# Optimization experiments

Measured on AMD Instinct MI355X. Metric: run time of the kernel, lower is better.

Reference implementation:

```python
import jax, jax.numpy as jnp
import numpy as np

NP, NA, H, K, TAU = 4096, 2048, 128, 5, 1.0
NODE_N = {'paper': NP, 'author': NA}
RELS = [('pp', 'paper', 'paper'), ('aa', 'author', 'author'),
        ('pa', 'paper', 'author'), ('ap', 'author', 'paper')]


def setup_inputs():
    key = jax.random.key(0)
    ks = jax.random.split(key, 32)
    f32 = jnp.float32
    def nrm(k, shape, scale=1.0):
        return jax.random.normal(k, shape, f32) * scale
    Epp, Eaa, Epa, Eap = 131072, 65536, 131072, 131072
    inp = {
        'x_paper': nrm(ks[0], (NP, H)),
        'x_author': nrm(ks[1], (NA, H)),
        'ei_pp': jax.random.randint(ks[2], (2, Epp), 0, NP, dtype=jnp.int32),
        'ei_aa': jax.random.randint(ks[3], (2, Eaa), 0, NA, dtype=jnp.int32),
        'ei_pa': jnp.stack([jax.random.randint(ks[4], (Epa,), 0, NP, dtype=jnp.int32),
                            jax.random.randint(ks[5], (Epa,), 0, NA, dtype=jnp.int32)]),
        'ei_ap': jnp.stack([jax.random.randint(ks[6], (Eap,), 0, NA, dtype=jnp.int32),
                            jax.random.randint(ks[7], (Eap,), 0, NP, dtype=jnp.int32)]),
        'batch_paper': jnp.zeros((NP,), jnp.int32),
        'batch_author': jnp.zeros((NA,), jnp.int32),
        'index': 7,
    }
    s = H ** -0.5
    i = 8
    for t in ('paper', 'author'):
        for l in (0, 1):
            inp['Wself_%s%d' % (t, l)] = nrm(ks[i], (H, H), s); i += 1
    for r, _, _ in RELS:
        for l in (0, 1):
            inp['W%s%d' % (r, l)] = nrm(ks[i], (H, H), s); i += 1
    for r in ('pp', 'aa'):
        inp['Wep1_%s' % r] = nrm(ks[i], (2 * H, 256), (2 * H) ** -0.5); i += 1
        inp['bep1_%s' % r] = jnp.zeros((256,), f32)
        inp['Wep2_%s' % r] = nrm(ks[i], (256, 2), 256 ** -0.5); i += 1
        inp['bep2_%s' % r] = jnp.zeros((2,), f32)
    inp['Wc'] = nrm(ks[i], (H, 5), s)
    inp['bc'] = jnp.zeros((5,), f32)
    return inp


def _mean_agg(msg, dst, n):
    s = jax.ops.segment_sum(msg, dst, num_segments=n)
    c = jax.ops.segment_sum(jnp.ones((msg.shape[0], 1), msg.dtype), dst, num_segments=n)
    return s / jnp.maximum(c, 1.0)


def _gnn(x, ei, p, single, edge_attn=None):
    # 2-layer relation-typed mean-aggregation hetero GNN.
    h = dict(x)
    for l in (0, 1):
        nh = {}
        for t in ('paper', 'author'):
            agg = h[t] @ p['Wself_%s%d' % (t, l)]
            for r, s_t, d_t in RELS:
                if d_t != t or (single and s_t != d_t):
                    continue
                src, dst = ei[r][0], ei[r][1]
                msg = h[s_t][src] @ p['W%s%d' % (r, l)]  # [E, H]
                if edge_attn is not None and r in edge_attn:
                    msg = msg * edge_attn[r][:, None]
                agg = agg + _mean_agg(msg, dst, NODE_N[t])
            nh[t] = jax.nn.relu(agg)
        h = nh
    return h


def _edge_pred(h, ei, p, r, t):
    src, dst = ei[r][0], ei[r][1]
    e = jnp.concatenate([h[t][src], h[t][dst]], axis=-1)  # [E, 2H]
    e = jax.nn.relu(e @ p['Wep1_%s' % r] + p['bep1_%s' % r])
    return e @ p['Wep2_%s' % r] + p['bep2_%s' % r]  # [E, 2]


def _gumbel_topk(logits, mask, k, tau, key):
    # Masked straight-through top-k gumbel-softmax (row-wise, hard=True).
    u = jax.random.uniform(key, logits.shape, logits.dtype, 1e-10, 1.0)
    g = -jnp.log(-jnp.log(u))
    y = jnp.where(mask, (logits + g) / tau, -1e9)
    soft = jax.nn.softmax(y, axis=-1)
    _, idx = jax.lax.top_k(soft, k)  # [N, k]
    rows = jnp.arange(logits.shape[0])[:, None]
    hard = jnp.zeros_like(soft).at[rows, idx].set(1.0)
    return hard - jax.lax.stop_gradient(soft) + soft


def _prune(h, ei, p, r, t, n, key):
    pred = _edge_pred(h, ei, p, r, t)[:, 0]
    src, dst = ei[r][0], ei[r][1]
    # sparse_coo_tensor(...).to_dense(): duplicates coalesce by sum
    A = jnp.zeros((n, n), pred.dtype).at[src, dst].add(pred)
    S = _gumbel_topk(A, A > 0, K, TAU, key)
    return S[src, dst]


def _forward(p, ints):
    x = {'paper': p['x_paper'], 'author': p['x_author']}
    ei = {'pp': ints['ei_pp'], 'aa': ints['ei_aa'], 'pa': ints['ei_pa'], 'ap': ints['ei_ap']}
    h1 = _gnn(x, ei, p, single=True)
    kpp, kaa = jax.random.split(jax.random.key(42))
    w_pp = _prune(h1, ei, p, 'pp', 'paper', NP, kpp)
    w_aa = _prune(h1, ei, p, 'aa', 'author', NA, kaa)
    h2 = _gnn(x, ei, p, single=False, edge_attn={'pp': w_pp, 'aa': w_aa})
    pool = h2['paper'][ints['index']].reshape(1, -1)
    y_hat = pool @ p['Wc'] + p['bc']
    return y_hat, w_pp, w_aa


def reference(x_paper, x_author, ei_pp, ei_aa, ei_pa, ei_ap, batch_paper, batch_author, index,
              Wself_paper0, Wself_paper1, Wself_author0, Wself_author1,
              Wpp0, Wpp1, Waa0, Waa1, Wpa0, Wpa1, Wap0, Wap1,
              Wep1_pp, bep1_pp, Wep2_pp, bep2_pp, Wep1_aa, bep1_aa, Wep2_aa, bep2_aa,
              Wc, bc):
    p = dict(x_paper=x_paper, x_author=x_author,
             Wself_paper0=Wself_paper0, Wself_paper1=Wself_paper1,
             Wself_author0=Wself_author0, Wself_author1=Wself_author1,
             Wpp0=Wpp0, Wpp1=Wpp1, Waa0=Waa0, Waa1=Waa1,
             Wpa0=Wpa0, Wpa1=Wpa1, Wap0=Wap0, Wap1=Wap1,
             Wep1_pp=Wep1_pp, bep1_pp=bep1_pp, Wep2_pp=Wep2_pp, bep2_pp=bep2_pp,
             Wep1_aa=Wep1_aa, bep1_aa=bep1_aa, Wep2_aa=Wep2_aa, bep2_aa=bep2_aa,
             Wc=Wc, bc=bc)
    ints = dict(ei_pp=ei_pp, ei_aa=ei_aa, ei_pa=ei_pa, ei_ap=ei_ap, index=index)
    return _forward(p, ints)
```

## Files before the change

### kernel.cpp

```cpp
#include <hip/hip_runtime.h>
#include <stdint.h>


namespace {

constexpr int NPn = 4096;
constexpr int NAn = 2048;
constexpr int Hh  = 128;
constexpr int EPPc = 131072;
constexpr int EAAc = 65536;
constexpr int KSEL = 5;
constexpr int BSLOT = 128;


__host__ __device__ static inline void tf2x32(uint32_t k0, uint32_t k1,
                                              uint32_t& x0, uint32_t& x1) {
  uint32_t ks2 = k0 ^ k1 ^ 0x1BD11BDAu;
  x0 += k0; x1 += k1;
#define TF_R(r) { x0 += x1; x1 = (x1 << (r)) | (x1 >> (32 - (r))); x1 ^= x0; }
  TF_R(13) TF_R(15) TF_R(26) TF_R(6)
  x0 += k1;  x1 += ks2 + 1u;
  TF_R(17) TF_R(29) TF_R(16) TF_R(24)
  x0 += ks2; x1 += k0 + 2u;
  TF_R(13) TF_R(15) TF_R(26) TF_R(6)
  x0 += k0;  x1 += k1 + 3u;
  TF_R(17) TF_R(29) TF_R(16) TF_R(24)
  x0 += k1;  x1 += ks2 + 4u;
  TF_R(13) TF_R(15) TF_R(26) TF_R(6)
  x0 += ks2; x1 += k0 + 5u;
#undef TF_R
}

__global__ __launch_bounds__(256) void scatter_kernel(
    const int* src_pp, const int* dst_pp, const int* src_aa, const int* dst_aa,
    const int* src_pa, const int* dst_pa, const int* src_ap, const int* dst_ap,
    int* cnt, int* entries)
{
  int i = blockIdx.x * 256 + threadIdx.x;
  int key, pl;
  if (i < 131072) {
    int e = i;
    key = 0 + dst_pp[e]; pl = (src_pp[e] << 18) | e;
  } else if (i < 196608) {
    int e = i - 131072;
    key = 4096 + dst_aa[e]; pl = (src_aa[e] << 16) | e;
  } else if (i < 327680) {
    int e = i - 196608;
    key = 6144 + dst_pa[e]; pl = src_pa[e];
  } else if (i < 458752) {
    int e = i - 327680;
    key = 8192 + dst_ap[e]; pl = src_ap[e];
  } else if (i < 589824) {
    int e = i - 458752;
    key = 12288 + src_pp[e]; pl = (dst_pp[e] << 18) | e;
  } else if (i < 655360) {
    int e = i - 589824;
    key = 16384 + src_aa[e]; pl = (dst_aa[e] << 16) | e;
  } else return;
  int pos = atomicAdd(&cnt[key], 1);
  if (pos < BSLOT) entries[key * BSLOT + pos] = pl;
}

struct FDesc {
  const float* gsrc; const float* wArr; int cntOff; int shift;
  float* Mout;
  const float* Aself; const float* W0; const float* W1;
  const float* A2;  const float* W2;
  float* C; int relu;
  const float* WP; float* P1; float* P2;
};
struct FArgs { FDesc d[4]; int bstart[5]; int nd; };

__global__ __launch_bounds__(256) void fused_layer(FArgs fa, const int* __restrict__ cnt,
                                                   const int* __restrict__ entries)
{
  extern __shared__ __align__(16) float lds[];
  float (*Xs)[128] = (float (*)[128])(lds);
  float (*Ms)[128] = (float (*)[128])(lds + 16 * 128);
  float (*Ws)[128] = (float (*)[128])(lds + 32 * 128);
  float (*Zs)[128] = (float (*)[128])(lds + 64 * 128);
  int blk = blockIdx.x, tid = threadIdx.x;
  int di = 0;
  while (di < fa.nd - 1 && blk >= fa.bstart[di + 1]) ++di;
  FDesc D = fa.d[di];
  bool isGemm = (D.W0 != nullptr);
  int node0 = (blk - fa.bstart[di]) * (isGemm ? 16 : 8);
  {
    int hw = tid >> 5;
    int fl = (tid & 31) << 2;
    int npass = isGemm ? 2 : 1;
    for (int ps = 0; ps < npass; ++ps) {
      int node = node0 + ps * 8 + hw;
      int deg = cnt[D.cntOff + node];
      const int* ent = entries + (size_t)(D.cntOff + node) * BSLOT;
      const float* h = D.gsrc;
      int sh = D.shift;
      float ax = 0.f, ay = 0.f, az = 0.f, aw = 0.f;
      if (D.wArr) {
        unsigned mask = (1u << sh) - 1u;
        int k = 0;
        for (; k + 3 < deg; k += 4) {
          unsigned p0 = (unsigned)ent[k], p1 = (unsigned)ent[k + 1];
          unsigned p2 = (unsigned)ent[k + 2], p3 = (unsigned)ent[k + 3];
          float w0 = D.wArr[p0 & mask], w1 = D.wArr[p1 & mask];
          float w2v = D.wArr[p2 & mask], w3 = D.wArr[p3 & mask];
          float4 v0, v1, v2, v3;
          if (w0 != 0.f) v0 = *(const float4*)&h[(size_t)(p0 >> sh) * Hh + fl];
          if (w1 != 0.f) v1 = *(const float4*)&h[(size_t)(p1 >> sh) * Hh + fl];
          if (w2v != 0.f) v2 = *(const float4*)&h[(size_t)(p2 >> sh) * Hh + fl];
          if (w3 != 0.f) v3 = *(const float4*)&h[(size_t)(p3 >> sh) * Hh + fl];
          if (w0 != 0.f) { ax += v0.x; ay += v0.y; az += v0.z; aw += v0.w; }
          if (w1 != 0.f) { ax += v1.x; ay += v1.y; az += v1.z; aw += v1.w; }
          if (w2v != 0.f) { ax += v2.x; ay += v2.y; az += v2.z; aw += v2.w; }
          if (w3 != 0.f) { ax += v3.x; ay += v3.y; az += v3.z; aw += v3.w; }
        }
        for (; k < deg; ++k) {
          unsigned pl = (unsigned)ent[k];
          float wt = D.wArr[pl & mask];
          if (wt != 0.f) {
            float4 v = *(const float4*)&h[(size_t)(pl >> sh) * Hh + fl];
            ax += v.x; ay += v.y; az += v.z; aw += v.w;
          }
        }
      } else {
        int k = 0;
        for (; k + 7 < deg; k += 8) {
          unsigned p0 = (unsigned)ent[k],     p1 = (unsigned)ent[k + 1];
          unsigned p2 = (unsigned)ent[k + 2], p3 = (unsigned)ent[k + 3];
          unsigned p4 = (unsigned)ent[k + 4], p5 = (unsigned)ent[k + 5];
          unsigned p6 = (unsigned)ent[k + 6], p7 = (unsigned)ent[k + 7];
          float4 v0 = *(const float4*)&h[(size_t)(p0 >> sh) * Hh + fl];
          float4 v1 = *(const float4*)&h[(size_t)(p1 >> sh) * Hh + fl];
          float4 v2 = *(const float4*)&h[(size_t)(p2 >> sh) * Hh + fl];
          float4 v3 = *(const float4*)&h[(size_t)(p3 >> sh) * Hh + fl];
          float4 v4 = *(const float4*)&h[(size_t)(p4 >> sh) * Hh + fl];
          float4 v5 = *(const float4*)&h[(size_t)(p5 >> sh) * Hh + fl];
          float4 v6 = *(const float4*)&h[(size_t)(p6 >> sh) * Hh + fl];
          float4 v7 = *(const float4*)&h[(size_t)(p7 >> sh) * Hh + fl];
          ax += v0.x; ay += v0.y; az += v0.z; aw += v0.w;
          ax += v1.x; ay += v1.y; az += v1.z; aw += v1.w;
          ax += v2.x; ay += v2.y; az += v2.z; aw += v2.w;
          ax += v3.x; ay += v3.y; az += v3.z; aw += v3.w;
          ax += v4.x; ay += v4.y; az += v4.z; aw += v4.w;
          ax += v5.x; ay += v5.y; az += v5.z; aw += v5.w;
          ax += v6.x; ay += v6.y; az += v6.z; aw += v6.w;
          ax += v7.x; ay += v7.y; az += v7.z; aw += v7.w;
        }
        for (; k < deg; ++k) {
          unsigned pl = (unsigned)ent[k];
          float4 v = *(const float4*)&h[(size_t)(pl >> sh) * Hh + fl];
          ax += v.x; ay += v.y; az += v.z; aw += v.w;
        }
      }
      float cd = fmaxf((float)deg, 1.0f);
      float4 o; o.x = ax / cd; o.y = ay / cd; o.z = az / cd; o.w = aw / cd;
      if (!isGemm) {
        *(float4*)&D.Mout[(size_t)node * Hh + fl] = o;
      } else {
        *(float4*)&Ms[ps * 8 + hw][fl] = o;
      }
    }
  }
  if (!isGemm) return;
  {
    int cq = (tid & 31) << 2;
    for (int q = 0; q < 2; ++q) {
      int rm = (tid >> 5) + q * 8;
      *(float4*)&Xs[rm][cq] = *(const float4*)&D.Aself[(size_t)(node0 + rm) * 128 + cq];
      if (D.A2)
        *(float4*)&Zs[rm][cq] = *(const float4*)&D.A2[(size_t)(node0 + rm) * 128 + cq];
    }
  }
  int rg = tid >> 5, nq = tid & 31;
  int r0 = rg * 2;
  float4 acc0 = {0.f, 0.f, 0.f, 0.f};
  float4 acc1 = {0.f, 0.f, 0.f, 0.f};
  int parts = D.A2 ? 3 : 2;
  for (int p = 0; p < parts; ++p) {
    const float* W = (p == 0) ? D.W0 : (p == 1) ? D.W1 : D.W2;
    for (int c = 0; c < 4; ++c) {
      __syncthreads();
      {
        int r = tid >> 3, f = (tid & 7) << 4;
        const float* srcp = &W[(size_t)(c * 32 + r) * 128 + f];
        *(float4*)&Ws[r][f]      = *(const float4*)&srcp[0];
        *(float4*)&Ws[r][f + 4]  = *(const float4*)&srcp[4];
        *(float4*)&Ws[r][f + 8]  = *(const float4*)&srcp[8];
        *(float4*)&Ws[r][f + 12] = *(const float4*)&srcp[12];
      }
      __syncthreads();
#define KCHUNK(AR)                                              \
      _Pragma("unroll")                                         \
      for (int k = 0; k < 32; ++k) {                            \
        float4 wv = *(const float4*)&Ws[k][nq << 2];            \
        float a0 = AR[r0][c * 32 + k];                          \
        float a1 = AR[r0 + 1][c * 32 + k];                      \
        acc0.x += a0 * wv.x; acc0.y += a0 * wv.y;               \
        acc0.z += a0 * wv.z; acc0.w += a0 * wv.w;               \
        acc1.x += a1 * wv.x; acc1.y += a1 * wv.y;               \
        acc1.z += a1 * wv.z; acc1.w += a1 * wv.w;               \
      }
      if (p == 0) { KCHUNK(Xs) } else if (p == 1) { KCHUNK(Ms) } else { KCHUNK(Zs) }
#undef KCHUNK
    }
  }
  if (D.relu) {
    acc0.x = fmaxf(acc0.x, 0.f); acc0.y = fmaxf(acc0.y, 0.f);
    acc0.z = fmaxf(acc0.z, 0.f); acc0.w = fmaxf(acc0.w, 0.f);
    acc1.x = fmaxf(acc1.x, 0.f); acc1.y = fmaxf(acc1.y, 0.f);
    acc1.z = fmaxf(acc1.z, 0.f); acc1.w = fmaxf(acc1.w, 0.f);
  }
  if (D.C) {
    *(float4*)&D.C[(size_t)(node0 + r0) * 128 + (nq << 2)]     = acc0;
    *(float4*)&D.C[(size_t)(node0 + r0 + 1) * 128 + (nq << 2)] = acc1;
  }
  if (D.WP == nullptr) return;
  __syncthreads();
  *(float4*)&Xs[r0][nq << 2]     = acc0;
  *(float4*)&Xs[r0 + 1][nq << 2] = acc1;
  __syncthreads();
  {
    int half = tid >> 7;
    int rgp = (tid >> 6) & 1;
    int c0 = (tid & 63) << 2;
    const float* Wb = D.WP + ((size_t)(half ? 128 : 0)) * 256 + c0;
    float* Pout = half ? D.P2 : D.P1;
    for (int q = 0; q < 2; ++q) {
      int rb = q * 8 + rgp * 4;
      float4 a_0 = {0,0,0,0}, a_1 = {0,0,0,0}, a_2 = {0,0,0,0}, a_3 = {0,0,0,0};
      for (int k = 0; k < 128; k += 2) {
        float4 w0 = *(const float4*)&Wb[(size_t)k * 256];
        float4 w1 = *(const float4*)&Wb[(size_t)(k + 1) * 256];
        float2 x0 = *(const float2*)&Xs[rb + 0][k];
        float2 x1 = *(const float2*)&Xs[rb + 1][k];
        float2 x2 = *(const float2*)&Xs[rb + 2][k];
        float2 x3 = *(const float2*)&Xs[rb + 3][k];
        a_0.x += x0.x * w0.x; a_0.y += x0.x * w0.y; a_0.z += x0.x * w0.z; a_0.w += x0.x * w0.w;
        a_0.x += x0.y * w1.x; a_0.y += x0.y * w1.y; a_0.z += x0.y * w1.z; a_0.w += x0.y * w1.w;
        a_1.x += x1.x * w0.x; a_1.y += x1.x * w0.y; a_1.z += x1.x * w0.z; a_1.w += x1.x * w0.w;
        a_1.x += x1.y * w1.x; a_1.y += x1.y * w1.y; a_1.z += x1.y * w1.z; a_1.w += x1.y * w1.w;
        a_2.x += x2.x * w0.x; a_2.y += x2.x * w0.y; a_2.z += x2.x * w0.z; a_2.w += x2.x * w0.w;
        a_2.x += x2.y * w1.x; a_2.y += x2.y * w1.y; a_2.z += x2.y * w1.z; a_2.w += x2.y * w1.w;
        a_3.x += x3.x * w0.x; a_3.y += x3.x * w0.y; a_3.z += x3.x * w0.z; a_3.w += x3.x * w0.w;
        a_3.x += x3.y * w1.x; a_3.y += x3.y * w1.y; a_3.z += x3.y * w1.z; a_3.w += x3.y * w1.w;
      }
      *(float4*)&Pout[(size_t)(node0 + rb + 0) * 256 + c0] = a_0;
      *(float4*)&Pout[(size_t)(node0 + rb + 1) * 256 + c0] = a_1;
      *(float4*)&Pout[(size_t)(node0 + rb + 2) * 256 + c0] = a_2;
      *(float4*)&Pout[(size_t)(node0 + rb + 3) * 256 + c0] = a_3;
    }
  }
}

__global__ __launch_bounds__(256) void row_topk(
    const float* __restrict__ P1pp, const float* __restrict__ P2pp,
    const float* __restrict__ b1pp, const float* __restrict__ W2pp,
    const float* __restrict__ b2pp,
    const float* __restrict__ P1aa, const float* __restrict__ P2aa,
    const float* __restrict__ b1aa, const float* __restrict__ W2aa,
    const float* __restrict__ b2aa,
    const int* __restrict__ cnt, const int* __restrict__ entries,
    float* __restrict__ w_pp, float* __restrict__ w_aa,
    uint32_t kpp0, uint32_t kpp1, uint32_t kaa0, uint32_t kaa1)
{
  __shared__ int   dS[4][128];
  __shared__ float pS[4][128];
  __shared__ int   sel5[4][KSEL];
  int blk = blockIdx.x, tid = threadIdx.x;
  int lane = tid & 63, wv = tid >> 6;
  int row, Ncols, shift;
  int co; unsigned mask;
  const float* P1; const float* P2; const float* b1; const float* W2; const float* b2;
  float* wout; uint32_t k0, k1;
  if (blk < NPn / 4) {
    row = blk * 4 + wv; Ncols = NPn; shift = 18; mask = 0x3FFFFu; co = 12288;
    P1 = P1pp; P2 = P2pp; b1 = b1pp; W2 = W2pp; b2 = b2pp;
    wout = w_pp; k0 = kpp0; k1 = kpp1;
  } else {
    row = (blk - NPn / 4) * 4 + wv; Ncols = NAn; shift = 16; mask = 0xFFFFu; co = 16384;
    P1 = P1aa; P2 = P2aa; b1 = b1aa; W2 = W2aa; b2 = b2aa;
    wout = w_aa; k0 = kaa0; k1 = kaa1;
  }
  const int* ent = entries + (size_t)(co + row) * BSLOT;
  int deg = cnt[co + row];
  int j = lane << 2;
  float4 p1v = *(const float4*)&P1[(size_t)row * 256 + j];
  float4 b1v = *(const float4*)&b1[j];
  float wa = W2[(j + 0) * 2], wb = W2[(j + 1) * 2];
  float wc = W2[(j + 2) * 2], wd = W2[(j + 3) * 2];
  float bias2 = b2[0];
  float pa = p1v.x, pb = p1v.y, pc = p1v.z, pd = p1v.w;
  float ba = b1v.x, bb = b1v.y, bc_ = b1v.z, bd = b1v.w;
#define SCORE(q) (fmaxf(pa + q.x + ba, 0.f) * wa + fmaxf(pb + q.y + bb, 0.f) * wb + \
                  fmaxf(pc + q.z + bc_, 0.f) * wc + fmaxf(pd + q.w + bd, 0.f) * wd)
  for (int k = 0; k < deg; k += 8) {
    int n = deg - k; if (n > 8) n = 8;
    unsigned pl0 = (unsigned)ent[k];
    unsigned pl1 = (n > 1) ? (unsigned)ent[k + 1] : pl0;
    unsigned pl2 = (n > 2) ? (unsigned)ent[k + 2] : pl0;
    unsigned pl3 = (n > 3) ? (unsigned)ent[k + 3] : pl0;
    unsigned pl4 = (n > 4) ? (unsigned)ent[k + 4] : pl0;
    unsigned pl5 = (n > 5) ? (unsigned)ent[k + 5] : pl0;
    unsigned pl6 = (n > 6) ? (unsigned)ent[k + 6] : pl0;
    unsigned pl7 = (n > 7) ? (unsigned)ent[k + 7] : pl0;
    int d0 = (int)(pl0 >> shift), d1 = (int)(pl1 >> shift);
    int d2 = (int)(pl2 >> shift), d3 = (int)(pl3 >> shift);
    int d4 = (int)(pl4 >> shift), d5 = (int)(pl5 >> shift);
    int d6 = (int)(pl6 >> shift), d7 = (int)(pl7 >> shift);
    float4 q0 = *(const float4*)&P2[(size_t)d0 * 256 + j];
    float4 q1 = *(const float4*)&P2[(size_t)d1 * 256 + j];
    float4 q2 = *(const float4*)&P2[(size_t)d2 * 256 + j];
    float4 q3 = *(const float4*)&P2[(size_t)d3 * 256 + j];
    float4 q4 = *(const float4*)&P2[(size_t)d4 * 256 + j];
    float4 q5 = *(const float4*)&P2[(size_t)d5 * 256 + j];
    float4 q6 = *(const float4*)&P2[(size_t)d6 * 256 + j];
    float4 q7 = *(const float4*)&P2[(size_t)d7 * 256 + j];
    float s0 = SCORE(q0), s1 = SCORE(q1), s2 = SCORE(q2), s3 = SCORE(q3);
    float s4 = SCORE(q4), s5 = SCORE(q5), s6 = SCORE(q6), s7 = SCORE(q7);
    for (int off = 32; off; off >>= 1) {
      s0 += __shfl_down(s0, off);
      s1 += __shfl_down(s1, off);
      s2 += __shfl_down(s2, off);
      s3 += __shfl_down(s3, off);
      s4 += __shfl_down(s4, off);
      s5 += __shfl_down(s5, off);
      s6 += __shfl_down(s6, off);
      s7 += __shfl_down(s7, off);
    }
    if (lane == 0) {
      dS[wv][k] = d0; pS[wv][k] = s0 + bias2;
      if (n > 1) { dS[wv][k + 1] = d1; pS[wv][k + 1] = s1 + bias2; }
      if (n > 2) { dS[wv][k + 2] = d2; pS[wv][k + 2] = s2 + bias2; }
      if (n > 3) { dS[wv][k + 3] = d3; pS[wv][k + 3] = s3 + bias2; }
      if (n > 4) { dS[wv][k + 4] = d4; pS[wv][k + 4] = s4 + bias2; }
      if (n > 5) { dS[wv][k + 5] = d5; pS[wv][k + 5] = s5 + bias2; }
      if (n > 6) { dS[wv][k + 6] = d6; pS[wv][k + 6] = s6 + bias2; }
      if (n > 7) { dS[wv][k + 7] = d7; pS[wv][k + 7] = s7 + bias2; }
    }
  }
#undef SCORE
  __syncthreads();
  if (deg > 0) {
    int   e0 = (lane < deg) ? dS[wv][lane] : -1;
    float q0v = (lane < deg) ? pS[wv][lane] : 0.f;
    bool  two = (deg > 64);
    int   e1 = -1; float q1v = 0.f;
    if (two && 64 + lane < deg) { e1 = dS[wv][64 + lane]; q1v = pS[wv][64 + lane]; }
    float a0 = 0.f, a1 = 0.f;
    bool lead0 = (e0 >= 0), lead1 = (e1 >= 0);
    for (int j2 = 0; j2 < deg; ++j2) {
      int bj; float bp;
      if (j2 < 64) { bj = __shfl(e0, j2); bp = __shfl(q0v, j2); }
      else         { bj = __shfl(e1, j2 - 64); bp = __shfl(q1v, j2 - 64); }
      if (e0 >= 0 && bj == e0) { a0 += bp; if (j2 < lane) lead0 = false; }
      if (e1 >= 0 && bj == e1) { a1 += bp; if (j2 < 64 + lane) lead1 = false; }
    }
    uint32_t rowbase = (uint32_t)row * (uint32_t)Ncols;
    float y0 = -1e9f, y1 = -1e9f;
    bool c0 = lead0 && (a0 > 0.f);
    if (c0) {
      uint32_t x0 = 0u, x1 = rowbase + (uint32_t)e0;
      tf2x32(k0, k1, x0, x1);
      uint32_t bits = x0 ^ x1;
      float fv = __uint_as_float((bits >> 9) | 0x3f800000u) - 1.0f;
      float u = fmaxf(1e-10f, fv + 1e-10f);
      y0 = a0 + (-logf(-logf(u)));
    }
    bool c1 = lead1 && (a1 > 0.f);
    if (c1) {
      uint32_t x0 = 0u, x1 = rowbase + (uint32_t)e1;
      tf2x32(k0, k1, x0, x1);
      uint32_t bits = x0 ^ x1;
      float fv = __uint_as_float((bits >> 9) | 0x3f800000u) - 1.0f;
      float u = fmaxf(1e-10f, fv + 1e-10f);
      y1 = a1 + (-logf(-logf(u)));
    }
    int cnt2 = __popcll(__ballot(c0)) + __popcll(__ballot(c1));
    int nsel = cnt2 < KSEL ? cnt2 : KSEL;
    for (int it = 0; it < nsel; ++it) {
      float best; int bc;
      if (y1 > y0 || (y1 == y0 && (unsigned)e1 < (unsigned)e0)) { best = y1; bc = e1; }
      else { best = y0; bc = e0; }
      for (int mm = 32; mm; mm >>= 1) {
        float ov = __shfl_xor(best, mm); int oc = __shfl_xor(bc, mm);
        if (ov > best || (ov == best && (unsigned)oc < (unsigned)bc)) { best = ov; bc = oc; }
      }
      if (lane == 0) sel5[wv][it] = bc;
      if (e0 == bc) y0 = -3.0e38f;
      if (e1 == bc) y1 = -3.0e38f;
    }
    if (nsel < KSEL && lane == 0) {
      int c = 0;
      for (int it = nsel; it < KSEL; ++it) {
        for (;;) {
          bool used = false;
          for (int q = 0; q < it; ++q) used |= (sel5[wv][q] == c);
          if (!used) break;
          ++c;
        }
        sel5[wv][it] = c++;
      }
    }
  }
  __syncthreads();
  for (int k = lane; k < deg; k += 64) {
    unsigned pl = (unsigned)ent[k];
    int d = (int)(pl >> shift);
    int e = (int)(pl & mask);
    float v = 0.f;
#pragma unroll
    for (int q = 0; q < KSEL; ++q) v = (sel5[wv][q] == d) ? 1.f : v;
    wout[e] = v;
  }
}

__global__ __launch_bounds__(128) void final_kernel(
    const float* __restrict__ hp, const float* __restrict__ ha,
    const int* __restrict__ idxPtr, const float* __restrict__ wpp,
    const int* __restrict__ cnt, const int* __restrict__ entries,
    const float* __restrict__ Wself, const float* __restrict__ Wpp,
    const float* __restrict__ Wap,
    const float* __restrict__ Wc, const float* __restrict__ bc,
    float* __restrict__ out)
{
  __shared__ float selfr[128], mpp[128], mapr[128], t[128];
  int tid = threadIdx.x;
  int idx = idxPtr[0];
  selfr[tid] = hp[(size_t)idx * 128 + tid];
  {
    int deg = cnt[idx];
    const int* ent = entries + (size_t)idx * BSLOT;
    float acc = 0.f;
    for (int k = 0; k < deg; ++k) {
      unsigned pl = (unsigned)ent[k];
      int s = (int)(pl >> 18);
      int e = (int)(pl & 0x3FFFFu);
      acc += wpp[e] * hp[(size_t)s * 128 + tid];
    }
    mpp[tid] = acc / fmaxf((float)deg, 1.0f);
  }
  {
    int deg = cnt[8192 + idx];
    const int* ent = entries + (size_t)(8192 + idx) * BSLOT;
    float acc = 0.f;
    for (int k = 0; k < deg; ++k) {
      int s = ent[k];
      acc += ha[(size_t)s * 128 + tid];
    }
    mapr[tid] = acc / fmaxf((float)deg, 1.0f);
  }
  __syncthreads();
  float s = 0.f;
  for (int m = 0; m < 128; ++m) {
    s += selfr[m] * Wself[m * 128 + tid] + mpp[m] * Wpp[m * 128 + tid] +
         mapr[m] * Wap[m * 128 + tid];
  }
  t[tid] = fmaxf(s, 0.f);
  __syncthreads();
  if (tid < 5) {
    float y = bc[tid];
    for (int k = 0; k < 128; ++k) y += t[k] * Wc[k * 5 + tid];
    out[tid] = y;
  }
}

}

extern "C" void kernel_launch(void* const* d_in, const int* in_sizes, int n_in,
                              void* d_out, int out_size, void* d_ws, size_t ws_size,
                              hipStream_t stream)
{
  (void)in_sizes; (void)n_in; (void)out_size; (void)ws_size;
  const float* x_p = (const float*)d_in[0];
  const float* x_a = (const float*)d_in[1];
  const int* ei_pp = (const int*)d_in[2];
  const int* ei_aa = (const int*)d_in[3];
  const int* ei_pa = (const int*)d_in[4];
  const int* ei_ap = (const int*)d_in[5];
  const int* idxPtr = (const int*)d_in[8];
  const float* Wself_p0 = (const float*)d_in[9];
  const float* Wself_p1 = (const float*)d_in[10];
  const float* Wself_a0 = (const float*)d_in[11];
  const float* Wself_a1 = (const float*)d_in[12];
  const float* Wpp0 = (const float*)d_in[13]; const float* Wpp1 = (const float*)d_in[14];
  const float* Waa0 = (const float*)d_in[15]; const float* Waa1 = (const float*)d_in[16];
  const float* Wpa0 = (const float*)d_in[17];
  const float* Wap0 = (const float*)d_in[19]; const float* Wap1 = (const float*)d_in[20];
  const float* Wep1_pp = (const float*)d_in[21]; const float* bep1_pp = (const float*)d_in[22];
  const float* Wep2_pp = (const float*)d_in[23]; const float* bep2_pp = (const float*)d_in[24];
  const float* Wep1_aa = (const float*)d_in[25]; const float* bep1_aa = (const float*)d_in[26];
  const float* Wep2_aa = (const float*)d_in[27]; const float* bep2_aa = (const float*)d_in[28];
  const float* Wc = (const float*)d_in[29]; const float* bc = (const float*)d_in[30];

  float* out = (float*)d_out;
  float* w_pp_out = out + 5;
  float* w_aa_out = out + 5 + EPPc;

  const int* src_pp = ei_pp;  const int* dst_pp = ei_pp + EPPc;
  const int* src_aa = ei_aa;  const int* dst_aa = ei_aa + EAAc;
  const int* src_pa = ei_pa;  const int* dst_pa = ei_pa + 131072;
  const int* src_ap = ei_ap;  const int* dst_ap = ei_ap + 131072;

  char* p = (char*)d_ws;
  auto alloc = [&](size_t bytes) -> void* {
    void* r = (void*)p;
    p += (bytes + 255) & ~(size_t)255;
    return r;
  };
  int* cnt     = (int*)alloc(18432 * sizeof(int));
  int* entries = (int*)alloc((size_t)18432 * BSLOT * sizeof(int));
  float* Map  = (float*)alloc((size_t)NPn * Hh * sizeof(float));
  float* Mpa  = (float*)alloc((size_t)NAn * Hh * sizeof(float));
  float* h1p0 = (float*)alloc((size_t)NPn * Hh * sizeof(float));
  float* h1a0 = (float*)alloc((size_t)NAn * Hh * sizeof(float));
  float* h2p0 = (float*)alloc((size_t)NPn * Hh * sizeof(float));
  float* h2a0 = (float*)alloc((size_t)NAn * Hh * sizeof(float));
  float* P1pp = (float*)alloc((size_t)NPn * 256 * sizeof(float));
  float* P2pp = (float*)alloc((size_t)NPn * 256 * sizeof(float));
  float* P1aa = (float*)alloc((size_t)NAn * 256 * sizeof(float));
  float* P2aa = (float*)alloc((size_t)NAn * 256 * sizeof(float));

  const int CO_PPD = 0, CO_AAD = 4096, CO_PAD = 6144, CO_APD = 8192;

  const size_t SH_NOZ = (size_t)64 * 128 * sizeof(float);
  const size_t SH_Z   = (size_t)80 * 128 * sizeof(float);

  hipMemsetAsync(cnt, 0, 18432 * sizeof(int), stream);
  scatter_kernel<<<2560, 256, 0, stream>>>(src_pp, dst_pp, src_aa, dst_aa,
                                           src_pa, dst_pa, src_ap, dst_ap,
                                           cnt, entries);

  {
    FArgs fa{};
    fa.d[0] = {x_p, nullptr, CO_PPD, 18, nullptr,
               x_p, Wself_p0, Wpp0, nullptr, nullptr, h1p0, 1,
               nullptr, nullptr, nullptr};
    fa.d[1] = {x_a, nullptr, CO_AAD, 16, nullptr,
               x_a, Wself_a0, Waa0, nullptr, nullptr, h1a0, 1,
               nullptr, nullptr, nullptr};
    fa.d[2] = {x_a, nullptr, CO_APD, 0, Map,
               nullptr, nullptr, nullptr, nullptr, nullptr, nullptr, 0,
               nullptr, nullptr, nullptr};
    fa.d[3] = {x_p, nullptr, CO_PAD, 0, Mpa,
               nullptr, nullptr, nullptr, nullptr, nullptr, nullptr, 0,
               nullptr, nullptr, nullptr};
    fa.bstart[0] = 0; fa.bstart[1] = 256; fa.bstart[2] = 384;
    fa.bstart[3] = 896; fa.bstart[4] = 1152; fa.nd = 4;
    fused_layer<<<1152, 256, SH_NOZ, stream>>>(fa, cnt, entries);
  }

  {
    FArgs fa{};
    fa.d[0] = {h1p0, nullptr, CO_PPD, 18, nullptr,
               h1p0, Wself_p1, Wpp1, nullptr, nullptr, nullptr, 1,
               Wep1_pp, P1pp, P2pp};
    fa.d[1] = {h1a0, nullptr, CO_AAD, 16, nullptr,
               h1a0, Wself_a1, Waa1, nullptr, nullptr, nullptr, 1,
               Wep1_aa, P1aa, P2aa};
    fa.bstart[0] = 0; fa.bstart[1] = 256; fa.bstart[2] = 384; fa.nd = 2;
    fused_layer<<<384, 256, SH_NOZ, stream>>>(fa, cnt, entries);
  }

  uint32_t kpp0, kpp1, kaa0, kaa1;
  { uint32_t a0 = 0, a1 = 0; tf2x32(0u, 42u, a0, a1); kpp0 = a0; kpp1 = a1; }
  { uint32_t a0 = 0, a1 = 1; tf2x32(0u, 42u, a0, a1); kaa0 = a0; kaa1 = a1; }

  row_topk<<<(NPn + NAn) / 4, 256, 0, stream>>>(P1pp, P2pp, bep1_pp, Wep2_pp, bep2_pp,
                                                P1aa, P2aa, bep1_aa, Wep2_aa, bep2_aa,
                                                cnt, entries, w_pp_out, w_aa_out,
                                                kpp0, kpp1, kaa0, kaa1);

  {
    FArgs fa{};
    fa.d[0] = {x_p, w_pp_out, CO_PPD, 18, nullptr,
               x_p, Wself_p0, Wpp0, Map, Wap0, h2p0, 1,
               nullptr, nullptr, nullptr};
    fa.d[1] = {x_a, w_aa_out, CO_AAD, 16, nullptr,
               x_a, Wself_a0, Waa0, Mpa, Wpa0, h2a0, 1,
               nullptr, nullptr, nullptr};
    fa.bstart[0] = 0; fa.bstart[1] = 256; fa.bstart[2] = 384; fa.nd = 2;
    fused_layer<<<384, 256, SH_Z, stream>>>(fa, cnt, entries);
  }

  final_kernel<<<1, 128, 0, stream>>>(h2p0, h2a0, idxPtr, w_pp_out,
                                      cnt, entries,
                                      Wself_p1, Wpp1, Wap1, Wc, bc, out);
}
```

Baseline: 342.4 us.

## Prefetch weight tiles into registers, vectorize A reads, and simplify dedup loop

The fused layer GEMM now loads the next 32-row weight chunk into registers while the current chunk is being used, which flattens the part/chunk loop into a single pipelined loop. The A-operand rows are read as float4 from a padded LDS layout (stride 132) to reduce LDS instruction count. In the Gumbel top-k dedup step, per-iteration shuffles are replaced with broadcast reads from LDS, and a single-half fast path is added for degree up to 64. Register pressure rises and the LDS footprint grows slightly.

```diff
diff --git a/kernel.cpp b/kernel.cpp
--- a/kernel.cpp
+++ b/kernel.cpp
@@ -11,6 +11,7 @@
 constexpr int EAAc = 65536;
 constexpr int KSEL = 5;
 constexpr int BSLOT = 128;
+constexpr int APAD = 132;
 
 
 __host__ __device__ static inline void tf2x32(uint32_t k0, uint32_t k1,
@@ -75,10 +76,10 @@
                                                    const int* __restrict__ entries)
 {
   extern __shared__ __align__(16) float lds[];
-  float (*Xs)[128] = (float (*)[128])(lds);
-  float (*Ms)[128] = (float (*)[128])(lds + 16 * 128);
-  float (*Ws)[128] = (float (*)[128])(lds + 32 * 128);
-  float (*Zs)[128] = (float (*)[128])(lds + 64 * 128);
+  float (*Ws)[128]  = (float (*)[128])(lds);
+  float (*Xs)[APAD] = (float (*)[APAD])(lds + 4096);
+  float (*Ms)[APAD] = (float (*)[APAD])(lds + 4096 + 16 * APAD);
+  float (*Zs)[APAD] = (float (*)[APAD])(lds + 4096 + 32 * APAD);
   int blk = blockIdx.x, tid = threadIdx.x;
   int di = 0;
   while (di < fa.nd - 1 && blk >= fa.bstart[di + 1]) ++di;
@@ -172,37 +173,65 @@
     }
   }
   int rg = tid >> 5, nq = tid & 31;
-  int r0 = rg * 2;
+  int m0 = rg * 2, m1 = m0 + 1;
+  int r = tid >> 3, f = (tid & 7) << 4;
   float4 acc0 = {0.f, 0.f, 0.f, 0.f};
   float4 acc1 = {0.f, 0.f, 0.f, 0.f};
   int parts = D.A2 ? 3 : 2;
-  for (int p = 0; p < parts; ++p) {
-    const float* W = (p == 0) ? D.W0 : (p == 1) ? D.W1 : D.W2;
-    for (int c = 0; c < 4; ++c) {
-      __syncthreads();
-      {
-        int r = tid >> 3, f = (tid & 7) << 4;
-        const float* srcp = &W[(size_t)(c * 32 + r) * 128 + f];
-        *(float4*)&Ws[r][f]      = *(const float4*)&srcp[0];
-        *(float4*)&Ws[r][f + 4]  = *(const float4*)&srcp[4];
-        *(float4*)&Ws[r][f + 8]  = *(const float4*)&srcp[8];
-        *(float4*)&Ws[r][f + 12] = *(const float4*)&srcp[12];
-      }
-      __syncthreads();
+  int T = parts * 4;
+  float4 g0, g1, g2, g3;
+  {
+    const float* srcp = &D.W0[(size_t)r * 128 + f];
+    g0 = *(const float4*)&srcp[0];
+    g1 = *(const float4*)&srcp[4];
+    g2 = *(const float4*)&srcp[8];
+    g3 = *(const float4*)&srcp[12];
+  }
+  for (int t = 0; t < T; ++t) {
+    __syncthreads();
+    *(float4*)&Ws[r][f]      = g0;
+    *(float4*)&Ws[r][f + 4]  = g1;
+    *(float4*)&Ws[r][f + 8]  = g2;
+    *(float4*)&Ws[r][f + 12] = g3;
+    if (t + 1 < T) {
+      int p2 = (t + 1) >> 2, ci = (t + 1) & 3;
+      const float* Wn = (p2 == 0) ? D.W0 : (p2 == 1) ? D.W1 : D.W2;
+      const float* srcp = &Wn[(size_t)(ci * 32 + r) * 128 + f];
+      g0 = *(const float4*)&srcp[0];
+      g1 = *(const float4*)&srcp[4];
+      g2 = *(const float4*)&srcp[8];
+      g3 = *(const float4*)&srcp[12];
+    }
+    __syncthreads();
+    int p = t >> 2, c = t & 3;
 #define KCHUNK(AR)                                              \
-      _Pragma("unroll")                                         \
-      for (int k = 0; k < 32; ++k) {                            \
-        float4 wv = *(const float4*)&Ws[k][nq << 2];            \
-        float a0 = AR[r0][c * 32 + k];                          \
-        float a1 = AR[r0 + 1][c * 32 + k];                      \
-        acc0.x += a0 * wv.x; acc0.y += a0 * wv.y;               \
-        acc0.z += a0 * wv.z; acc0.w += a0 * wv.w;               \
-        acc1.x += a1 * wv.x; acc1.y += a1 * wv.y;               \
-        acc1.z += a1 * wv.z; acc1.w += a1 * wv.w;               \
-      }
-      if (p == 0) { KCHUNK(Xs) } else if (p == 1) { KCHUNK(Ms) } else { KCHUNK(Zs) }
+    _Pragma("unroll")                                           \
+    for (int k4 = 0; k4 < 32; k4 += 4) {                        \
+      float4 a0v = *(const float4*)&AR[m0][c * 32 + k4];        \
+      float4 a1v = *(const float4*)&AR[m1][c * 32 + k4];        \
+      float4 w0 = *(const float4*)&Ws[k4 + 0][nq << 2];         \
+      float4 w1 = *(const float4*)&Ws[k4 + 1][nq << 2];         \
+      float4 w2v = *(const float4*)&Ws[k4 + 2][nq << 2];        \
+      float4 w3 = *(const float4*)&Ws[k4 + 3][nq << 2];         \
+      acc0.x += a0v.x * w0.x; acc0.y += a0v.x * w0.y;           \
+      acc0.z += a0v.x * w0.z; acc0.w += a0v.x * w0.w;           \
+      acc0.x += a0v.y * w1.x; acc0.y += a0v.y * w1.y;           \
+      acc0.z += a0v.y * w1.z; acc0.w += a0v.y * w1.w;           \
+      acc0.x += a0v.z * w2v.x; acc0.y += a0v.z * w2v.y;         \
+      acc0.z += a0v.z * w2v.z; acc0.w += a0v.z * w2v.w;         \
+      acc0.x += a0v.w * w3.x; acc0.y += a0v.w * w3.y;           \
+      acc0.z += a0v.w * w3.z; acc0.w += a0v.w * w3.w;           \
+      acc1.x += a1v.x * w0.x; acc1.y += a1v.x * w0.y;           \
+      acc1.z += a1v.x * w0.z; acc1.w += a1v.x * w0.w;           \
+      acc1.x += a1v.y * w1.x; acc1.y += a1v.y * w1.y;           \
+      acc1.z += a1v.y * w1.z; acc1.w += a1v.y * w1.w;           \
+      acc1.x += a1v.z * w2v.x; acc1.y += a1v.z * w2v.y;         \
+      acc1.z += a1v.z * w2v.z; acc1.w += a1v.z * w2v.w;         \
+      acc1.x += a1v.w * w3.x; acc1.y += a1v.w * w3.y;           \
+      acc1.z += a1v.w * w3.z; acc1.w += a1v.w * w3.w;           \
+    }
+    if (p == 0) { KCHUNK(Xs) } else if (p == 1) { KCHUNK(Ms) } else { KCHUNK(Zs) }
 #undef KCHUNK
-    }
   }
   if (D.relu) {
     acc0.x = fmaxf(acc0.x, 0.f); acc0.y = fmaxf(acc0.y, 0.f);
@@ -211,22 +240,22 @@
     acc1.z = fmaxf(acc1.z, 0.f); acc1.w = fmaxf(acc1.w, 0.f);
   }
   if (D.C) {
-    *(float4*)&D.C[(size_t)(node0 + r0) * 128 + (nq << 2)]     = acc0;
-    *(float4*)&D.C[(size_t)(node0 + r0 + 1) * 128 + (nq << 2)] = acc1;
+    *(float4*)&D.C[(size_t)(node0 + m0) * 128 + (nq << 2)] = acc0;
+    *(float4*)&D.C[(size_t)(node0 + m1) * 128 + (nq << 2)] = acc1;
   }
   if (D.WP == nullptr) return;
   __syncthreads();
-  *(float4*)&Xs[r0][nq << 2]     = acc0;
-  *(float4*)&Xs[r0 + 1][nq << 2] = acc1;
+  *(float4*)&Xs[m0][nq << 2] = acc0;
+  *(float4*)&Xs[m1][nq << 2] = acc1;
   __syncthreads();
   {
     int half = tid >> 7;
-    int rgp = (tid >> 6) & 1;
+    int rg2 = (tid >> 6) & 1;
     int c0 = (tid & 63) << 2;
     const float* Wb = D.WP + ((size_t)(half ? 128 : 0)) * 256 + c0;
     float* Pout = half ? D.P2 : D.P1;
     for (int q = 0; q < 2; ++q) {
-      int rb = q * 8 + rgp * 4;
+      int rb = q * 8 + rg2 * 4;
       float4 a_0 = {0,0,0,0}, a_1 = {0,0,0,0}, a_2 = {0,0,0,0}, a_3 = {0,0,0,0};
       for (int k = 0; k < 128; k += 2) {
         float4 w0 = *(const float4*)&Wb[(size_t)k * 256];
@@ -342,18 +371,24 @@
   __syncthreads();
   if (deg > 0) {
     int   e0 = (lane < deg) ? dS[wv][lane] : -1;
-    float q0v = (lane < deg) ? pS[wv][lane] : 0.f;
     bool  two = (deg > 64);
-    int   e1 = -1; float q1v = 0.f;
-    if (two && 64 + lane < deg) { e1 = dS[wv][64 + lane]; q1v = pS[wv][64 + lane]; }
+    int   e1 = -1;
+    if (two && 64 + lane < deg) e1 = dS[wv][64 + lane];
     float a0 = 0.f, a1 = 0.f;
     bool lead0 = (e0 >= 0), lead1 = (e1 >= 0);
-    for (int j2 = 0; j2 < deg; ++j2) {
-      int bj; float bp;
-      if (j2 < 64) { bj = __shfl(e0, j2); bp = __shfl(q0v, j2); }
-      else         { bj = __shfl(e1, j2 - 64); bp = __shfl(q1v, j2 - 64); }
-      if (e0 >= 0 && bj == e0) { a0 += bp; if (j2 < lane) lead0 = false; }
-      if (e1 >= 0 && bj == e1) { a1 += bp; if (j2 < 64 + lane) lead1 = false; }
+    if (!two) {
+#pragma unroll 4
+      for (int j2 = 0; j2 < deg; ++j2) {
+        int bj = dS[wv][j2]; float bp = pS[wv][j2];
+        if (bj == e0) { a0 += bp; if (j2 < lane) lead0 = false; }
+      }
+    } else {
+#pragma unroll 2
+      for (int j2 = 0; j2 < deg; ++j2) {
+        int bj = dS[wv][j2]; float bp = pS[wv][j2];
+        if (e0 >= 0 && bj == e0) { a0 += bp; if (j2 < lane) lead0 = false; }
+        if (e1 >= 0 && bj == e1) { a1 += bp; if (j2 < 64 + lane) lead1 = false; }
+      }
     }
     uint32_t rowbase = (uint32_t)row * (uint32_t)Ncols;
     float y0 = -1e9f, y1 = -1e9f;
@@ -522,8 +557,8 @@
 
   const int CO_PPD = 0, CO_AAD = 4096, CO_PAD = 6144, CO_APD = 8192;
 
-  const size_t SH_NOZ = (size_t)64 * 128 * sizeof(float);
-  const size_t SH_Z   = (size_t)80 * 128 * sizeof(float);
+  const size_t SH_NOZ = (size_t)(4096 + 32 * APAD) * sizeof(float);
+  const size_t SH_Z   = (size_t)(4096 + 48 * APAD) * sizeof(float);
 
   hipMemsetAsync(cnt, 0, 18432 * sizeof(int), stream);
   scatter_kernel<<<2560, 256, 0, stream>>>(src_pp, dst_pp, src_aa, dst_aa,
```

Measured after the change: 338.1 us. No clear change (-1.3%).
